# Performance work log

Hardware: AMD Instinct MI355X
Metric: run time of the kernel (lower is better)

The kernel has to match this reference:

```python
import jax, jax.numpy as jnp
from jax import lax
import numpy as np

B, H, W = 2, 48, 48
C_IN, C_OUT = 96, 192
D_INNER, N_STATE, DT_RANK, K = 192, 16, 6, 4  # VMamba: expand=2, d_state=16, dt_rank=ceil(C/16)
EPS = 1e-5


def setup_inputs() -> dict:
    ks = jax.random.split(jax.random.key(0), 16)
    s = 0.02
    r = lambda k, sh, sc=s: jax.random.normal(k, sh, jnp.float32) * sc
    d, N, R = D_INNER, N_STATE, DT_RANK
    return {
        "x": jax.random.normal(ks[0], (B, C_IN, H, W), jnp.float32),
        "ln_g": jnp.ones((C_IN,), jnp.float32),
        "ln_b": jnp.zeros((C_IN,), jnp.float32),
        "in_proj_w": r(ks[1], (2 * d, C_IN)),
        "dwconv_w": r(ks[2], (d, 1, 3, 3)),
        "dwconv_b": jnp.zeros((d,), jnp.float32),
        "x_proj_w": r(ks[3], (K, R + 2 * N, d)),
        "dt_w": r(ks[4], (K, d, R)),
        "dt_b": r(ks[5], (K, d), 0.1),
        "A_logs": jnp.tile(jnp.log(jnp.arange(1, N + 1, dtype=jnp.float32)), (K, d, 1)),
        "Ds": jnp.ones((K, d), jnp.float32),
        "out_norm_g": jnp.ones((d,), jnp.float32),
        "out_norm_b": jnp.zeros((d,), jnp.float32),
        "out_proj_w": r(ks[6], (C_IN, d)),
        "w1": r(ks[7], (C_OUT, C_IN, 1, 1)),
        "b1": jnp.zeros((C_OUT,), jnp.float32),
        "w31": r(ks[8], (C_OUT, C_IN, 3, 3)),
        "b31": jnp.zeros((C_OUT,), jnp.float32),
        "w32": r(ks[9], (C_OUT, C_IN, 3, 3)),
        "b32": jnp.zeros((C_OUT,), jnp.float32),
        "w33": r(ks[10], (C_OUT, C_OUT, 3, 3)),
        "b33": jnp.zeros((C_OUT,), jnp.float32),
        "bn_g": jnp.ones((3 * C_OUT,), jnp.float32),
        "bn_b": jnp.zeros((3 * C_OUT,), jnp.float32),
        "bn_m": r(ks[11], (3 * C_OUT,), 0.1),
        "bn_v": jax.random.uniform(ks[12], (3 * C_OUT,), jnp.float32) + 0.5,
        "prelu_a": jnp.float32(0.25),
    }


def _layernorm(x, g, b):
    m = jnp.mean(x, -1, keepdims=True)
    v = jnp.var(x, -1, keepdims=True)
    return (x - m) * lax.rsqrt(v + EPS) * g + b


def _conv(x, w, b, stride, pad, groups=1):
    y = lax.conv_general_dilated(x, w, (stride, stride), [(pad, pad), (pad, pad)],
                                 dimension_numbers=("NCHW", "OIHW", "NCHW"),
                                 feature_group_count=groups)
    return y + b[None, :, None, None]


def _ss2d(x, in_proj_w, dwconv_w, dwconv_b, x_proj_w, dt_w, dt_b, A_logs, Ds,
          out_norm_g, out_norm_b, out_proj_w):
    # x: (B, H, W, C)
    Bb, Hh, Ww, C = x.shape
    d, N, R = D_INNER, N_STATE, DT_RANK
    L = Hh * Ww
    xz = jnp.einsum("bhwc,ec->bhwe", x, in_proj_w)  # (B,H,W,2d)
    xin, z = jnp.split(xz, 2, axis=-1)
    xc = jnp.transpose(xin, (0, 3, 1, 2))           # (B,d,H,W)
    xc = jax.nn.silu(_conv(xc, dwconv_w, dwconv_b, 1, 1, groups=d))
    # 4 scan directions: row-major, col-major, and their reverses
    x_flat = xc.reshape(Bb, d, L)
    x_t = jnp.transpose(xc, (0, 1, 3, 2)).reshape(Bb, d, L)
    xs = jnp.stack([x_flat, x_t, x_flat[:, :, ::-1], x_t[:, :, ::-1]], axis=1)  # (B,K,d,L)
    x_dbl = jnp.einsum("bkdl,kcd->bkcl", xs, x_proj_w)
    dts, Bs, Cs = x_dbl[:, :, :R], x_dbl[:, :, R:R + N], x_dbl[:, :, R + N:]
    delta = jax.nn.softplus(jnp.einsum("bkrl,kdr->bkdl", dts, dt_w) + dt_b[None, :, :, None])
    A = -jnp.exp(A_logs)                                   # (K,d,N)
    dA = jnp.exp(jnp.einsum("bkdl,kdn->lbkdn", delta, A))  # (L,B,K,d,N)
    dBu = jnp.einsum("bkdl,bknl,bkdl->lbkdn", delta, Bs, xs)
    Cseq = jnp.transpose(Cs, (3, 0, 1, 2))                 # (L,B,K,N)

    def step(h, inp):
        dA_t, dBu_t, c_t = inp
        h = dA_t * h + dBu_t
        return h, jnp.einsum("bkdn,bkn->bkd", h, c_t)

    h0 = jnp.zeros((Bb, K, d, N), x.dtype)
    _, ys = lax.scan(step, h0, (dA, dBu, Cseq))            # ys: (L,B,K,d)
    ys = jnp.transpose(ys, (1, 2, 3, 0)) + xs * Ds[None, :, :, None]  # (B,K,d,L)

    def t_back(a):  # undo the HW transpose of col-major scans
        return jnp.transpose(a.reshape(Bb, d, Ww, Hh), (0, 1, 3, 2)).reshape(Bb, d, L)

    y = ys[:, 0] + ys[:, 2, :, ::-1] + t_back(ys[:, 1]) + t_back(ys[:, 3, :, ::-1])
    y = _layernorm(jnp.transpose(y, (0, 2, 1)), out_norm_g, out_norm_b).reshape(Bb, Hh, Ww, d)
    y = y * jax.nn.silu(z)
    return jnp.einsum("bhwd,cd->bhwc", y, out_proj_w)


def reference(x, ln_g, ln_b, in_proj_w, dwconv_w, dwconv_b, x_proj_w, dt_w, dt_b,
              A_logs, Ds, out_norm_g, out_norm_b, out_proj_w,
              w1, b1, w31, b31, w32, b32, w33, b33,
              bn_g, bn_b, bn_m, bn_v, prelu_a):
    # VSSBlock: residual + SS2D on LayerNorm'd NHWC features
    x_nhwc = jnp.transpose(x, (0, 2, 3, 1))
    x_nhwc = x_nhwc + _ss2d(_layernorm(x_nhwc, ln_g, ln_b), in_proj_w, dwconv_w,
                            dwconv_b, x_proj_w, dt_w, dt_b, A_logs, Ds,
                            out_norm_g, out_norm_b, out_proj_w)
    xm = jnp.transpose(x_nhwc, (0, 3, 1, 2))  # (B,C,H,W)
    # multi-branch stride-2 downsample
    x1 = _conv(xm, w1, b1, 2, 0)
    x2 = _conv(xm, w31, b31, 2, 1)
    x3 = _conv(_conv(xm, w32, b32, 2, 1), w33, b33, 1, 1)
    out = jnp.concatenate([x1, x2, x3], axis=1)  # (B, 3*C_OUT, H/2, W/2)
    # BatchNorm2d (inference, running stats) + PReLU(single param)
    out = (out - bn_m[None, :, None, None]) * lax.rsqrt(bn_v + EPS)[None, :, None, None] \
          * bn_g[None, :, None, None] + bn_b[None, :, None, None]
    return jnp.where(out > 0, out, prelu_a * out)
```

## Files before the change

### kernel.cpp

```cpp
#include <hip/hip_runtime.h>
#include <math.h>

#define BB_ 2
#define HH 48
#define WW 48
#define LL 2304
#define CIN 96
#define DD 192
#define KK 4
#define NN 16
#define RR 6
#define NCH 96
#define LC 24
#define COUT 192
#define OH 24
#define OW 24
#define OHW 576
#define NPX 1152
#define NTOT 4608
#define EPSF 1e-5f

typedef __attribute__((ext_vector_type(8))) short bf16x8;
typedef __attribute__((ext_vector_type(4))) float f32x4;

__device__ __forceinline__ short f2bf(float f) {
  unsigned u = __float_as_uint(f);
  unsigned r = (u + 0x7fffu + ((u >> 16) & 1u)) >> 16;
  return (short)r;
}

__global__ __launch_bounds__(256) void k_prep(const float* __restrict__ x,
                                              const float* __restrict__ g,
                                              const float* __restrict__ b,
                                              const float* __restrict__ inw,
                                              const float* __restrict__ xpw,
                                              const float* __restrict__ w31,
                                              const float* __restrict__ w32,
                                              const float* __restrict__ w33,
                                              const float* __restrict__ w1,
                                              const float* __restrict__ wout,
                                              float* __restrict__ stats,
                                              float* __restrict__ WgT,
                                              float* __restrict__ sWg,
                                              float* __restrict__ sWb,
                                              short* __restrict__ At3p,
                                              short* __restrict__ At1b,
                                              short* __restrict__ At2b,
                                              short* __restrict__ woutb) {
  int bx = blockIdx.x;
  int tid = threadIdx.x;
  if (bx < 72) {
    int bb = bx / 36; int l0 = (bx % 36) * 64;
    int p = tid >> 2, q = tid & 3;
    int l = l0 + p;
    const float* xp = x + bb * CIN * LL + l;
    float s = 0.f, ss = 0.f;
    for (int c = q; c < CIN; c += 4) { float v = xp[c * LL]; s += v; ss += v * v; }
    s += __shfl_xor(s, 1, 64); s += __shfl_xor(s, 2, 64);
    ss += __shfl_xor(ss, 1, 64); ss += __shfl_xor(ss, 2, 64);
    if (q == 0) {
      float m = s / CIN; float var = ss / CIN - m * m;
      stats[(bb * LL + l) * 2 + 0] = m;
      stats[(bb * LL + l) * 2 + 1] = rsqrtf(var + EPSF);
    }
  } else if (bx == 72) {
    for (int e = tid; e < 2 * DD; e += 256) {
      float swg = 0.f, swb = 0.f;
      for (int c = 0; c < CIN; c++) {
        float w = inw[e * CIN + c];
        float wg = w * g[c];
        WgT[c * 384 + e] = wg;
        swg += wg; swb += w * b[c];
      }
      sWg[e] = swg; sWb[e] = swb;
    }
  } else if (bx < 217) {
    int idx = (bx - 73) * 256 + tid;
    if (idx < 4 * 48 * 192) {
      int m = idx / 192, d = idx - m * 192;
      int kd = m / 48, r = m - kd * 48;
      At3p[idx] = (r < 38) ? f2bf(xpw[(kd * 38 + r) * 192 + d]) : (short)0;
    }
  } else if (bx < 2161) {
    int i = (bx - 217) * 256 + tid;
    if (i < 497664) {
      float v;
      if (i < 165888) v = w31[i];
      else if (i < 331776) v = w32[i - 165888];
      else {
        int k = i % 864; int m = i / 864 - 384;
        v = (k % 9 == 4) ? w1[m * 96 + k / 9] : 0.f;
      }
      At1b[i] = f2bf(v);
    }
  } else if (bx < 3457) {
    int i = (bx - 2161) * 256 + tid;
    if (i < 331776) At2b[i] = f2bf(w33[i]);
  } else {
    int i = (bx - 3457) * 256 + tid;
    if (i < 18432) woutb[i] = f2bf(wout[i]);
  }
}

__global__ __launch_bounds__(256) void k_dwconv(const float* __restrict__ xin,
                                                const float* __restrict__ wdw,
                                                const float* __restrict__ bdw,
                                                float* __restrict__ xs,
                                                short* __restrict__ xsb) {
  __shared__ float vt[32 * 50];
  int bid = blockIdx.x;
  int bb = bid / 288; int r = bid % 288; int dg = r / 72; int tile = r % 72;
  int l0 = tile * 32;
  int d0 = dg * 48;
  for (int i = threadIdx.x; i < 32 * 48; i += 256) {
    int lj = i & 31, dl = i >> 5;
    int d = d0 + dl;
    int l = l0 + lj;
    int h = l / WW, w = l % WW;
    const float* xp = xin + (bb * DD + d) * LL;
    const float* wq = wdw + d * 9;
    float acc = bdw[d];
#pragma unroll
    for (int kh = 0; kh < 3; kh++) {
      int ih = h + kh - 1; if (ih < 0 || ih >= HH) continue;
#pragma unroll
      for (int kw = 0; kw < 3; kw++) {
        int iw = w + kw - 1; if (iw < 0 || iw >= WW) continue;
        acc += xp[ih * WW + iw] * wq[kh * 3 + kw];
      }
    }
    float v = acc / (1.f + __expf(-acc));
    vt[lj * 50 + dl] = v;
  }
  __syncthreads();
  for (int j = threadIdx.x; j < 32 * 48; j += 256) {
    int lj = j / 48, dl = j - lj * 48;
    int d = d0 + dl;
    int l = l0 + lj;
    int h = l / WW, w = l % WW;
    int lt = w * HH + h;
    float v = vt[lj * 50 + dl];
    xs[((size_t)(bb * 2 + 0) * LL + l) * DD + d] = v;
    xs[((size_t)(bb * 2 + 1) * LL + lt) * DD + d] = v;
    xsb[((size_t)bb * LL + l) * DD + d] = f2bf(v);
  }
}

__global__ __launch_bounds__(256) void k_xprojF(const short* __restrict__ At3p,
                                                const short* __restrict__ xsb,
                                                const float* __restrict__ dtw,
                                                const float* __restrict__ dtb,
                                                float* __restrict__ Bsb,
                                                float* __restrict__ Csb,
                                                float* __restrict__ delta) {
  __shared__ short As[48][40];
  __shared__ short Bs[64][40];
  __shared__ float ct[38][65];
  int bid = blockIdx.x;
  int kd = bid / 72; int tile = bid % 72;
  int pg0 = tile * 64;
  int bb = pg0 / LL;
  int lbase = pg0 - bb * LL;
  int tid = threadIdx.x;
  int lane = tid & 63;
  int wvn = tid >> 6;
  int row16 = lane & 15;
  int kg = lane >> 4;
  f32x4 acc[3];
#pragma unroll
  for (int j = 0; j < 3; j++) acc[j] = (f32x4){0.f, 0.f, 0.f, 0.f};
  int sm = tid >> 2, sk8 = (tid & 3) * 8;
  for (int ks = 0; ks < 192; ks += 32) {
    if (tid < 192)
      *(bf16x8*)&As[sm][sk8] =
          *(const bf16x8*)&At3p[(size_t)(kd * 48 + sm) * 192 + ks + sk8];
    *(bf16x8*)&Bs[sm][sk8] =
        *(const bf16x8*)&xsb[(size_t)(pg0 + sm) * 192 + ks + sk8];
    __syncthreads();
    bf16x8 b = *(const bf16x8*)&Bs[wvn * 16 + row16][kg * 8];
#pragma unroll
    for (int j = 0; j < 3; j++) {
      bf16x8 a = *(const bf16x8*)&As[j * 16 + row16][kg * 8];
      acc[j] = __builtin_amdgcn_mfma_f32_16x16x32_bf16(a, b, acc[j], 0, 0, 0);
    }
    __syncthreads();
  }
#pragma unroll
  for (int j = 0; j < 3; j++) {
    int rowb = j * 16 + kg * 4;
    int col = wvn * 16 + row16;
#pragma unroll
    for (int i = 0; i < 4; i++)
      if (rowb + i < 38) ct[rowb + i][col] = acc[j][i];
  }
  __syncthreads();
  for (int i = tid; i < 64 * 16; i += 256) {
    int lj = i >> 4, n = i & 15;
    int l = lbase + lj; int h = l / WW, w = l - h * WW; int lt = w * HH + h;
    int pos = (kd == 0) ? l : (kd == 1) ? lt : (kd == 2) ? (LL - 1 - l) : (LL - 1 - lt);
    size_t base = ((size_t)(bb * 4 + kd) * LL + pos) * NN + n;
    Bsb[base] = ct[6 + n][lj];
    Csb[base] = ct[22 + n][lj];
  }
  for (int i = tid; i < 64 * 192; i += 256) {
    int lj = i / 192, d = i - lj * 192;
    int l = lbase + lj; int h = l / WW, w = l - h * WW; int lt = w * HH + h;
    int pos = (kd == 0) ? l : (kd == 1) ? lt : (kd == 2) ? (LL - 1 - l) : (LL - 1 - lt);
    const float* wd = dtw + (kd * DD + d) * RR;
    float a2 = dtb[kd * DD + d];
#pragma unroll
    for (int r = 0; r < RR; r++) a2 += wd[r] * ct[r][lj];
    float sp = a2 > 20.f ? a2 : log1pf(__expf(a2));
    delta[((size_t)(bb * 4 + kd) * LL + pos) * DD + d] = sp;
  }
}

__global__ __launch_bounds__(192) void k_scan1(const float* __restrict__ delta,
                                               const float* __restrict__ xs,
                                               const float* __restrict__ Bsb,
                                               const float* __restrict__ A_logs,
                                               float* __restrict__ Pbuf,
                                               float* __restrict__ Sbuf) {
  __shared__ float Bls[LC * NN];
  int bid = blockIdx.x;
  int c = bid % NCH; int bk = bid / NCH; int k = bk & 3; int bb = bk >> 2;
  int t0 = c * LC;
  int d = threadIdx.x;
  const float* bp = Bsb + ((size_t)bk * LL + t0) * NN;
  for (int i = d; i < LC * NN; i += 192) Bls[i] = bp[i];
  float A[NN];
  {
    const float4* ap = (const float4*)(A_logs + (k * DD + d) * NN);
#pragma unroll
    for (int j = 0; j < 4; j++) {
      float4 a4 = ap[j];
      A[4 * j + 0] = -__expf(a4.x); A[4 * j + 1] = -__expf(a4.y);
      A[4 * j + 2] = -__expf(a4.z); A[4 * j + 3] = -__expf(a4.w);
    }
  }
  bool seq = true;
#pragma unroll
  for (int n = 0; n < NN; n++) seq = seq && (fabsf(A[n] + (float)(n + 1)) < 1e-3f);
  float h[NN];
#pragma unroll
  for (int n = 0; n < NN; n++) h[n] = 0.f;
  float sd = 0.f;
  __syncthreads();
  const float* dp = delta + ((size_t)bk * LL + t0) * DD + d;
  const float* xpb = xs + ((size_t)(bb * 2 + (k & 1)) * LL) * DD + d;
  const float* xp; int xstep;
  if (k < 2) { xp = xpb + (size_t)t0 * DD; xstep = DD; }
  else       { xp = xpb + (size_t)(LL - 1 - t0) * DD; xstep = -DD; }
#pragma unroll 2
  for (int t = 0; t < LC; ++t) {
    float dt = dp[t * DD];
    float xv = xp[t * xstep];
    float u = dt * xv;
    sd += dt;
    float dA[NN];
    if (seq) {
      float q = __expf(-dt);
      float q2 = q * q, q4 = q2 * q2, q8 = q4 * q4;
      dA[0] = q; dA[1] = q2; dA[2] = q2 * q; dA[3] = q4;
      dA[4] = q4 * q; dA[5] = q4 * q2; dA[6] = q4 * dA[2]; dA[7] = q8;
      dA[8] = q8 * q; dA[9] = q8 * q2; dA[10] = q8 * dA[2]; dA[11] = q8 * q4;
      dA[12] = q8 * dA[4]; dA[13] = q8 * dA[5]; dA[14] = q8 * dA[6]; dA[15] = q8 * q8;
    } else {
#pragma unroll
      for (int n = 0; n < NN; n++) dA[n] = __expf(dt * A[n]);
    }
    const float4* b4 = (const float4*)&Bls[t * NN];
#pragma unroll
    for (int j = 0; j < 4; j++) {
      float4 bv = b4[j];
      h[4 * j + 0] = dA[4 * j + 0] * h[4 * j + 0] + u * bv.x;
      h[4 * j + 1] = dA[4 * j + 1] * h[4 * j + 1] + u * bv.y;
      h[4 * j + 2] = dA[4 * j + 2] * h[4 * j + 2] + u * bv.z;
      h[4 * j + 3] = dA[4 * j + 3] * h[4 * j + 3] + u * bv.w;
    }
  }
  int chn = (bk * DD + d) * NN;
  float* pp = Pbuf + (size_t)c * 24576 + chn;
  float* sp = Sbuf + (size_t)c * 24576 + chn;
#pragma unroll
  for (int n = 0; n < NN; n++) { pp[n] = __expf(A[n] * sd); sp[n] = h[n]; }
}

__global__ __launch_bounds__(256) void k_scan2(const float* __restrict__ Pbuf,
                                               const float* __restrict__ Sbuf,
                                               float* __restrict__ Hinit) {
  int idx = blockIdx.x * 256 + threadIdx.x;
  float h = 0.f;
  for (int c = 0; c < NCH; c++) {
    Hinit[(size_t)c * 24576 + idx] = h;
    h = Pbuf[(size_t)c * 24576 + idx] * h + Sbuf[(size_t)c * 24576 + idx];
  }
}

__global__ __launch_bounds__(192) void k_scan3(const float* __restrict__ delta,
                                               const float* __restrict__ xs,
                                               const float* __restrict__ Bsb,
                                               const float* __restrict__ Csb,
                                               const float* __restrict__ A_logs,
                                               const float* __restrict__ Ds,
                                               const float* __restrict__ Hinit,
                                               float* __restrict__ ys) {
  __shared__ float Bls[LC * NN];
  __shared__ float Cls[LC * NN];
  int bid = blockIdx.x;
  int c = bid % NCH; int bk = bid / NCH; int k = bk & 3; int bb = bk >> 2;
  int t0 = c * LC;
  int d = threadIdx.x;
  const float* bp = Bsb + ((size_t)bk * LL + t0) * NN;
  const float* cp = Csb + ((size_t)bk * LL + t0) * NN;
  for (int i = d; i < LC * NN; i += 192) { Bls[i] = bp[i]; Cls[i] = cp[i]; }
  float A[NN];
  {
    const float4* ap = (const float4*)(A_logs + (k * DD + d) * NN);
#pragma unroll
    for (int j = 0; j < 4; j++) {
      float4 a4 = ap[j];
      A[4 * j + 0] = -__expf(a4.x); A[4 * j + 1] = -__expf(a4.y);
      A[4 * j + 2] = -__expf(a4.z); A[4 * j + 3] = -__expf(a4.w);
    }
  }
  bool seq = true;
#pragma unroll
  for (int n = 0; n < NN; n++) seq = seq && (fabsf(A[n] + (float)(n + 1)) < 1e-3f);
  float Dv = Ds[k * DD + d];
  float h[NN];
  {
    const float4* hp = (const float4*)(Hinit + (size_t)c * 24576 + (bk * DD + d) * NN);
#pragma unroll
    for (int j = 0; j < 4; j++) {
      float4 h4 = hp[j];
      h[4 * j + 0] = h4.x; h[4 * j + 1] = h4.y;
      h[4 * j + 2] = h4.z; h[4 * j + 3] = h4.w;
    }
  }
  __syncthreads();
  const float* dp = delta + ((size_t)bk * LL + t0) * DD + d;
  const float* xpb = xs + ((size_t)(bb * 2 + (k & 1)) * LL) * DD + d;
  const float* xp; int xstep;
  if (k < 2) { xp = xpb + (size_t)t0 * DD; xstep = DD; }
  else       { xp = xpb + (size_t)(LL - 1 - t0) * DD; xstep = -DD; }
  float* yp = ys + ((size_t)bk * LL + t0) * DD + d;
#pragma unroll 2
  for (int t = 0; t < LC; ++t) {
    float dt = dp[t * DD];
    float xv = xp[t * xstep];
    float u = dt * xv;
    float y = 0.f;
    float dA[NN];
    if (seq) {
      float q = __expf(-dt);
      float q2 = q * q, q4 = q2 * q2, q8 = q4 * q4;
      dA[0] = q; dA[1] = q2; dA[2] = q2 * q; dA[3] = q4;
      dA[4] = q4 * q; dA[5] = q4 * q2; dA[6] = q4 * dA[2]; dA[7] = q8;
      dA[8] = q8 * q; dA[9] = q8 * q2; dA[10] = q8 * dA[2]; dA[11] = q8 * q4;
      dA[12] = q8 * dA[4]; dA[13] = q8 * dA[5]; dA[14] = q8 * dA[6]; dA[15] = q8 * q8;
    } else {
#pragma unroll
      for (int n = 0; n < NN; n++) dA[n] = __expf(dt * A[n]);
    }
    const float4* b4 = (const float4*)&Bls[t * NN];
    const float4* c4 = (const float4*)&Cls[t * NN];
#pragma unroll
    for (int j = 0; j < 4; j++) {
      float4 bv = b4[j];
      float4 cc = c4[j];
      h[4 * j + 0] = dA[4 * j + 0] * h[4 * j + 0] + u * bv.x;
      h[4 * j + 1] = dA[4 * j + 1] * h[4 * j + 1] + u * bv.y;
      h[4 * j + 2] = dA[4 * j + 2] * h[4 * j + 2] + u * bv.z;
      h[4 * j + 3] = dA[4 * j + 3] * h[4 * j + 3] + u * bv.w;
      y += h[4 * j + 0] * cc.x + h[4 * j + 1] * cc.y
         + h[4 * j + 2] * cc.z + h[4 * j + 3] * cc.w;
    }
    yp[t * DD] = y + Dv * xv;
  }
}

__global__ __launch_bounds__(256) void k_combineF(const float* __restrict__ ys,
                                                  const float* __restrict__ z,
                                                  const float* __restrict__ ong,
                                                  const float* __restrict__ onb,
                                                  const short* __restrict__ Wbf,
                                                  const float* __restrict__ x,
                                                  float* __restrict__ xm) {
  __shared__ float yt[32 * 194];
  __shared__ unsigned Wlu[96 * 98];
  int bx = blockIdx.x; int bb = bx / 72; int l0 = (bx % 72) * 32;
  int tid = threadIdx.x;
  const unsigned* Wu = (const unsigned*)Wbf;
  for (int i = tid; i < 96 * 96; i += 256) {
    int e = i / 96, d2 = i - e * 96;
    Wlu[e * 98 + d2] = Wu[i];
  }
  for (int i = tid; i < 32 * DD; i += 256) {
    int p = i / DD, d = i - p * DD;
    int l = l0 + p; int h = l / WW, w = l - h * WW;
    int t1 = w * HH + h;
    float v = ys[(((size_t)bb * KK + 0) * LL + l) * DD + d]
            + ys[(((size_t)bb * KK + 1) * LL + t1) * DD + d]
            + ys[(((size_t)bb * KK + 2) * LL + (LL - 1 - l)) * DD + d]
            + ys[(((size_t)bb * KK + 3) * LL + (LL - 1 - t1)) * DD + d];
    yt[p * 194 + d] = v;
  }
  __syncthreads();
  int p = tid >> 3, q = tid & 7;
  int l = l0 + p;
  float s = 0.f, ss = 0.f;
  for (int d = q * 24; d < q * 24 + 24; d++) { float v = yt[p * 194 + d]; s += v; ss += v * v; }
  s += __shfl_xor(s, 1, 64); s += __shfl_xor(s, 2, 64); s += __shfl_xor(s, 4, 64);
  ss += __shfl_xor(ss, 1, 64); ss += __shfl_xor(ss, 2, 64); ss += __shfl_xor(ss, 4, 64);
  float m = s / DD, var = ss / DD - m * m;
  float rr = rsqrtf(var + EPSF);
  const float* zp = z + (bb * LL + l) * DD;
  for (int d = q * 24; d < q * 24 + 24; d++) {
    float v = (yt[p * 194 + d] - m) * rr * ong[d] + onb[d];
    float zv = zp[d];
    yt[p * 194 + d] = v * zv / (1.f + __expf(-zv));
  }
  __syncthreads();
  float acc[12];
#pragma unroll
  for (int j = 0; j < 12; j++) acc[j] = 0.f;
  for (int d2 = 0; d2 < 96; d2++) {
    float2 y2 = *(float2*)&yt[p * 194 + 2 * d2];
#pragma unroll
    for (int j = 0; j < 12; j++) {
      unsigned wv = Wlu[(q * 12 + j) * 98 + d2];
      float wlo = __uint_as_float(wv << 16);
      float whi = __uint_as_float(wv & 0xffff0000u);
      acc[j] += y2.x * wlo + y2.y * whi;
    }
  }
#pragma unroll
  for (int j = 0; j < 12; j++) {
    int e = q * 12 + j;
    size_t off = ((size_t)bb * CIN + e) * LL + l;
    xm[off] = x[off] + acc[j];
  }
}

template<int MT, int KTOT, int KCHUNK, int CI, int IH, int STRIDE>
__global__ __launch_bounds__(256) void k_cgemm_mfma(const short* __restrict__ Abf,
                                                    const float* __restrict__ SRC,
                                                    float* __restrict__ Cout) {
  __shared__ short As[64][40];
  __shared__ short Bs[64][40];
  int n0 = blockIdx.x * 64;
  int m0 = blockIdx.y * 64;
  int kz = blockIdx.z;
  int k0 = kz * KCHUNK;
  int tid = threadIdx.x;
  int lane = tid & 63;
  int wv = tid >> 6;
  int row16 = lane & 15;
  int kg = lane >> 4;
  int sm = tid >> 2;
  int sk8 = (tid & 3) * 8;
  int n = n0 + sm;
  int bb = n / OHW; int rem = n - bb * OHW;
  int oh = rem / OW, ow = rem - oh * OW;
  f32x4 acc[4];
#pragma unroll
  for (int i = 0; i < 4; i++) acc[i] = (f32x4){0.f, 0.f, 0.f, 0.f};
  for (int ks = 0; ks < KCHUNK; ks += 32) {
    *(bf16x8*)&As[sm][sk8] =
        *(const bf16x8*)&Abf[(size_t)(m0 + sm) * KTOT + k0 + ks + sk8];
    bf16x8 bvv;
#pragma unroll
    for (int j = 0; j < 8; j++) {
      int k = k0 + ks + sk8 + j;
      int ci = k / 9; int r9 = k - ci * 9;
      int kh = r9 / 3, kw = r9 - kh * 3;
      int ih = STRIDE * oh + kh - 1;
      int iw = STRIDE * ow + kw - 1;
      float v = (ih >= 0 && ih < IH && iw >= 0 && iw < IH)
              ? SRC[((size_t)(bb * CI + ci) * IH + ih) * IH + iw] : 0.f;
      bvv[j] = f2bf(v);
    }
    *(bf16x8*)&Bs[sm][sk8] = bvv;
    __syncthreads();
    bf16x8 a = *(const bf16x8*)&As[wv * 16 + row16][kg * 8];
#pragma unroll
    for (int tn = 0; tn < 4; tn++) {
      bf16x8 b = *(const bf16x8*)&Bs[tn * 16 + row16][kg * 8];
      acc[tn] = __builtin_amdgcn_mfma_f32_16x16x32_bf16(a, b, acc[tn], 0, 0, 0);
    }
    __syncthreads();
  }
#pragma unroll
  for (int tn = 0; tn < 4; tn++) {
    int col = n0 + tn * 16 + row16;
    int rowb = m0 + wv * 16 + kg * 4;
#pragma unroll
    for (int i = 0; i < 4; i++)
      Cout[((size_t)kz * MT + rowb + i) * NPX + col] = acc[tn][i];
  }
}

template<int MT, int KD>
__global__ __launch_bounds__(256) void k_gemmF(const float* __restrict__ At,
                                               const float* __restrict__ Bm,
                                               int ldb, int boffB,
                                               float* __restrict__ C0,
                                               int ldc, int boffC,
                                               const float* __restrict__ a0,
                                               const float* __restrict__ a1,
                                               const float* __restrict__ a2,
                                               float* __restrict__ a3) {
  __shared__ float As[16][64];
  __shared__ float Bs[16][64];
  int n0 = blockIdx.x * 64;
  int m0 = blockIdx.y * 64;
  int bb = blockIdx.z;
  const float* B = Bm + (size_t)bb * boffB;
  int tid = threadIdx.x;
  int lr = tid >> 4;
  int lc = (tid & 15) * 4;
  int tm = tid >> 4;
  int tn = tid & 15;
  float acc[4][4] = {};
  for (int ks = 0; ks < KD; ks += 16) {
    *(float4*)&As[lr][lc] = *(const float4*)&At[(ks + lr) * MT + m0 + lc];
    *(float4*)&Bs[lr][lc] = *(const float4*)&B[(size_t)(ks + lr) * ldb + n0 + lc];
    __syncthreads();
#pragma unroll
    for (int kk = 0; kk < 16; kk++) {
      float4 a = *(float4*)&As[kk][tm * 4];
      float4 b = *(float4*)&Bs[kk][tn * 4];
      acc[0][0] += a.x * b.x; acc[0][1] += a.x * b.y; acc[0][2] += a.x * b.z; acc[0][3] += a.x * b.w;
      acc[1][0] += a.y * b.x; acc[1][1] += a.y * b.y; acc[1][2] += a.y * b.z; acc[1][3] += a.y * b.w;
      acc[2][0] += a.z * b.x; acc[2][1] += a.z * b.y; acc[2][2] += a.z * b.z; acc[2][3] += a.z * b.w;
      acc[3][0] += a.w * b.x; acc[3][1] += a.w * b.y; acc[3][2] += a.w * b.z; acc[3][3] += a.w * b.w;
    }
    __syncthreads();
  }
  int n = n0 + tn * 4;
  float m_[4], r_[4];
#pragma unroll
  for (int j = 0; j < 4; j++) {
    m_[j] = a0[((size_t)bb * LL + n + j) * 2];
    r_[j] = a0[((size_t)bb * LL + n + j) * 2 + 1];
  }
#pragma unroll
  for (int i = 0; i < 4; i++) {
    int e = m0 + tm * 4 + i;
    float swg = a1[e], swb = a2[e];
    float v0 = r_[0] * (acc[i][0] - m_[0] * swg) + swb;
    float v1 = r_[1] * (acc[i][1] - m_[1] * swg) + swb;
    float v2 = r_[2] * (acc[i][2] - m_[2] * swg) + swb;
    float v3 = r_[3] * (acc[i][3] - m_[3] * swg) + swb;
    if (e < DD) {
      float4 v = {v0, v1, v2, v3};
      *(float4*)&C0[(size_t)bb * boffC + (size_t)e * ldc + n] = v;
    } else {
      a3[((size_t)bb * LL + n + 0) * DD + (e - DD)] = v0;
      a3[((size_t)bb * LL + n + 1) * DD + (e - DD)] = v1;
      a3[((size_t)bb * LL + n + 2) * DD + (e - DD)] = v2;
      a3[((size_t)bb * LL + n + 3) * DD + (e - DD)] = v3;
    }
  }
}

__global__ __launch_bounds__(256) void k_reduce1(const float* __restrict__ Cp1,
                                                 const float* __restrict__ b1,
                                                 const float* __restrict__ b31,
                                                 const float* __restrict__ b32,
                                                 const float* __restrict__ bn_g,
                                                 const float* __restrict__ bn_b,
                                                 const float* __restrict__ bn_m,
                                                 const float* __restrict__ bn_v,
                                                 const float* __restrict__ prelu_a,
                                                 float* __restrict__ out,
                                                 float* __restrict__ t3) {
  int idx = blockIdx.x * 256 + threadIdx.x;
  if (idx >= 576 * NPX) return;
  int m = idx / NPX, n = idx % NPX;
  float s = 0.f;
#pragma unroll
  for (int c = 0; c < 3; c++) s += Cp1[(size_t)c * 576 * NPX + idx];
  int bb = n / OHW, o = n % OHW;
  if (m < 192) {
    s += b31[m];
    int cc = 192 + m;
    float scale = rsqrtf(bn_v[cc] + EPSF) * bn_g[cc];
    float v = s * scale + (bn_b[cc] - bn_m[cc] * scale);
    float a = prelu_a[0];
    out[((size_t)bb * 576 + cc) * OHW + o] = v > 0.f ? v : a * v;
  } else if (m < 384) {
    s += b32[m - 192];
    t3[((size_t)bb * COUT + (m - 192)) * OHW + o] = s;
  } else {
    s += b1[m - 384];
    int cc = m - 384;
    float scale = rsqrtf(bn_v[cc] + EPSF) * bn_g[cc];
    float v = s * scale + (bn_b[cc] - bn_m[cc] * scale);
    float a = prelu_a[0];
    out[((size_t)bb * 576 + cc) * OHW + o] = v > 0.f ? v : a * v;
  }
}

__global__ __launch_bounds__(256) void k_reduce2(const float* __restrict__ Cp2,
                                                 const float* __restrict__ b33,
                                                 const float* __restrict__ bn_g,
                                                 const float* __restrict__ bn_b,
                                                 const float* __restrict__ bn_m,
                                                 const float* __restrict__ bn_v,
                                                 const float* __restrict__ prelu_a,
                                                 float* __restrict__ out) {
  int idx = blockIdx.x * 256 + threadIdx.x;
  if (idx >= 192 * NPX) return;
  int m = idx / NPX, n = idx % NPX;
  float s = b33[m];
#pragma unroll
  for (int c = 0; c < 6; c++) s += Cp2[(size_t)c * 192 * NPX + idx];
  int bb = n / OHW, o = n % OHW;
  int cc = 384 + m;
  float scale = rsqrtf(bn_v[cc] + EPSF) * bn_g[cc];
  float v = s * scale + (bn_b[cc] - bn_m[cc] * scale);
  float a = prelu_a[0];
  out[((size_t)bb * 576 + cc) * OHW + o] = v > 0.f ? v : a * v;
}

extern "C" void kernel_launch(void* const* d_in, const int* in_sizes, int n_in,
                              void* d_out, int out_size, void* d_ws, size_t ws_size,
                              hipStream_t stream) {
  const float* x        = (const float*)d_in[0];
  const float* ln_g     = (const float*)d_in[1];
  const float* ln_b     = (const float*)d_in[2];
  const float* in_proj_w= (const float*)d_in[3];
  const float* dwconv_w = (const float*)d_in[4];
  const float* dwconv_b = (const float*)d_in[5];
  const float* x_proj_w = (const float*)d_in[6];
  const float* dt_w     = (const float*)d_in[7];
  const float* dt_b     = (const float*)d_in[8];
  const float* A_logs   = (const float*)d_in[9];
  const float* Ds       = (const float*)d_in[10];
  const float* out_norm_g = (const float*)d_in[11];
  const float* out_norm_b = (const float*)d_in[12];
  const float* out_proj_w = (const float*)d_in[13];
  const float* w1  = (const float*)d_in[14];
  const float* b1  = (const float*)d_in[15];
  const float* w31 = (const float*)d_in[16];
  const float* b31 = (const float*)d_in[17];
  const float* w32 = (const float*)d_in[18];
  const float* b32 = (const float*)d_in[19];
  const float* w33 = (const float*)d_in[20];
  const float* b33 = (const float*)d_in[21];
  const float* bn_g = (const float*)d_in[22];
  const float* bn_b = (const float*)d_in[23];
  const float* bn_m = (const float*)d_in[24];
  const float* bn_v = (const float*)d_in[25];
  const float* prelu_a = (const float*)d_in[26];

  float* ws = (float*)d_ws;
  float* stats = ws + 0;
  float* WgT   = ws + 16384;
  float* sWg   = ws + 65536;
  float* sWb   = ws + 66048;
  short* At3p  = (short*)(ws + 98304);
  short* At1b  = (short*)(ws + 147456);
  short* At2b  = (short*)(ws + 397312);
  short* woutb = (short*)(ws + 565248);
  float* xin   = ws + 2097152;
  float* z     = ws + 3145728;
  float* xs    = ws + 4194304;
  short* xsb   = (short*)(ws + 6291456);
  float* delta = ws + 10485760;
  float* Bsb   = ws + 14155776;
  float* Csb   = ws + 14680064;
  float* Pbuf  = ws + 15728640;
  float* Sbuf  = ws + 18874368;
  float* Hinit = ws + 22020096;
  float* ys    = ws + 25165824;
  float* xm    = ws + 29360128;
  float* t3    = ws + 30408704;
  float* Cp1   = ws + 31457280;
  float* Cp2   = ws + 33554432;
  float* out = (float*)d_out;

  k_prep<<<3529, 256, 0, stream>>>(x, ln_g, ln_b, in_proj_w, x_proj_w,
                                   w31, w32, w33, w1, out_proj_w,
                                   stats, WgT, sWg, sWb, At3p, At1b, At2b, woutb);
  k_gemmF<384, 96><<<dim3(36, 6, 2), 256, 0, stream>>>(
      WgT, x, LL, CIN * LL, xin, LL, DD * LL, stats, sWg, sWb, z);
  k_dwconv<<<576, 256, 0, stream>>>(xin, dwconv_w, dwconv_b, xs, xsb);
  k_xprojF<<<288, 256, 0, stream>>>(At3p, xsb, dt_w, dt_b, Bsb, Csb, delta);
  k_scan1<<<768, 192, 0, stream>>>(delta, xs, Bsb, A_logs, Pbuf, Sbuf);
  k_scan2<<<96, 256, 0, stream>>>(Pbuf, Sbuf, Hinit);
  k_scan3<<<768, 192, 0, stream>>>(delta, xs, Bsb, Csb, A_logs, Ds, Hinit, ys);
  k_combineF<<<144, 256, 0, stream>>>(ys, z, out_norm_g, out_norm_b, woutb, x, xm);
  k_cgemm_mfma<576, 864, 288, CIN, HH, 2><<<dim3(18, 9, 3), 256, 0, stream>>>(
      At1b, xm, Cp1);
  k_reduce1<<<2592, 256, 0, stream>>>(Cp1, b1, b31, b32, bn_g, bn_b, bn_m, bn_v,
                                      prelu_a, out, t3);
  k_cgemm_mfma<192, 1728, 288, COUT, OH, 1><<<dim3(18, 3, 6), 256, 0, stream>>>(
      At2b, t3, Cp2);
  k_reduce2<<<864, 256, 0, stream>>>(Cp2, b33, bn_g, bn_b, bn_m, bn_v, prelu_a, out);
}
```

Before: 190.7 us.

## Move in_proj to bf16 MFMA, halve combine tile, unroll chunk scan

Replaces the fp32 SIMT in_proj GEMM with a bf16 MFMA kernel. The weights are stored as bf16 and the prep kernel gains extra blocks that transpose x to pixel-major bf16. The combine kernel now uses 16-pixel tiles, doubling its grid to 288 blocks for better occupancy. The inter-chunk scan loop is unrolled by 4. Rounding in_proj inputs to bf16 lowers precision, and the extra transpose pass costs memory traffic.

Measured after the change: 190.7 us. Within noise of the previous version (-0.0%).

```diff
diff --git a/kernel.cpp b/kernel.cpp
--- a/kernel.cpp
+++ b/kernel.cpp
@@ -40,13 +40,15 @@
                                               const float* __restrict__ w1,
                                               const float* __restrict__ wout,
                                               float* __restrict__ stats,
-                                              float* __restrict__ WgT,
+                                              short* __restrict__ WgTb,
                                               float* __restrict__ sWg,
                                               float* __restrict__ sWb,
                                               short* __restrict__ At3p,
                                               short* __restrict__ At1b,
                                               short* __restrict__ At2b,
-                                              short* __restrict__ woutb) {
+                                              short* __restrict__ woutb,
+                                              short* __restrict__ xb) {
+  __shared__ float tile[32][33];
   int bx = blockIdx.x;
   int tid = threadIdx.x;
   if (bx < 72) {
@@ -69,7 +71,7 @@
       for (int c = 0; c < CIN; c++) {
         float w = inw[e * CIN + c];
         float wg = w * g[c];
-        WgT[c * 384 + e] = wg;
+        WgTb[e * CIN + c] = f2bf(wg);
         swg += wg; swb += w * b[c];
       }
       sWg[e] = swg; sWb[e] = swb;
@@ -96,9 +98,70 @@
   } else if (bx < 3457) {
     int i = (bx - 2161) * 256 + tid;
     if (i < 331776) At2b[i] = f2bf(w33[i]);
-  } else {
+  } else if (bx < 3529) {
     int i = (bx - 3457) * 256 + tid;
     if (i < 18432) woutb[i] = f2bf(wout[i]);
+  } else {
+    int tt = bx - 3529;
+    int bb = tt / 216; int r2 = tt % 216;
+    int ct = r2 / 72, lt = r2 % 72;
+    int c0 = ct * 32, l0 = lt * 32;
+    int r = tid >> 5, cc = tid & 31;
+    for (int rr = r; rr < 32; rr += 8)
+      tile[rr][cc] = x[(size_t)bb * CIN * LL + (c0 + rr) * LL + l0 + cc];
+    __syncthreads();
+    for (int rr = r; rr < 32; rr += 8)
+      xb[((size_t)bb * LL + l0 + rr) * CIN + c0 + cc] = f2bf(tile[cc][rr]);
+  }
+}
+
+__global__ __launch_bounds__(256) void k_inprojM(const short* __restrict__ WgTb,
+                                                 const short* __restrict__ xb,
+                                                 const float* __restrict__ stats,
+                                                 const float* __restrict__ sWg,
+                                                 const float* __restrict__ sWb,
+                                                 float* __restrict__ xin,
+                                                 float* __restrict__ z) {
+  __shared__ short As[64][40];
+  __shared__ short Bs[64][40];
+  int n0 = blockIdx.x * 64;
+  int m0 = blockIdx.y * 64;
+  int tid = threadIdx.x;
+  int lane = tid & 63;
+  int wv = tid >> 6;
+  int row16 = lane & 15;
+  int kg = lane >> 4;
+  int sm = tid >> 2;
+  int sk8 = (tid & 3) * 8;
+  f32x4 acc[4];
+#pragma unroll
+  for (int i = 0; i < 4; i++) acc[i] = (f32x4){0.f, 0.f, 0.f, 0.f};
+#pragma unroll
+  for (int ks = 0; ks < 96; ks += 32) {
+    *(bf16x8*)&As[sm][sk8] = *(const bf16x8*)&WgTb[(size_t)(m0 + sm) * CIN + ks + sk8];
+    *(bf16x8*)&Bs[sm][sk8] = *(const bf16x8*)&xb[(size_t)(n0 + sm) * CIN + ks + sk8];
+    __syncthreads();
+    bf16x8 a = *(const bf16x8*)&As[wv * 16 + row16][kg * 8];
+#pragma unroll
+    for (int tn = 0; tn < 4; tn++) {
+      bf16x8 b = *(const bf16x8*)&Bs[tn * 16 + row16][kg * 8];
+      acc[tn] = __builtin_amdgcn_mfma_f32_16x16x32_bf16(a, b, acc[tn], 0, 0, 0);
+    }
+    __syncthreads();
+  }
+#pragma unroll
+  for (int tn = 0; tn < 4; tn++) {
+    int px = n0 + tn * 16 + row16;
+    int bb = px / LL, l = px - bb * LL;
+    float mm = stats[px * 2], rr = stats[px * 2 + 1];
+    int rowb = m0 + wv * 16 + kg * 4;
+#pragma unroll
+    for (int i = 0; i < 4; i++) {
+      int e = rowb + i;
+      float v = rr * (acc[tn][i] - mm * sWg[e]) + sWb[e];
+      if (e < DD) xin[((size_t)bb * DD + e) * LL + l] = v;
+      else z[(size_t)px * DD + (e - DD)] = v;
+    }
   }
 }
 
@@ -291,6 +354,7 @@
                                                float* __restrict__ Hinit) {
   int idx = blockIdx.x * 256 + threadIdx.x;
   float h = 0.f;
+#pragma unroll 4
   for (int c = 0; c < NCH; c++) {
     Hinit[(size_t)c * 24576 + idx] = h;
     h = Pbuf[(size_t)c * 24576 + idx] * h + Sbuf[(size_t)c * 24576 + idx];
@@ -387,16 +451,16 @@
                                                   const short* __restrict__ Wbf,
                                                   const float* __restrict__ x,
                                                   float* __restrict__ xm) {
-  __shared__ float yt[32 * 194];
+  __shared__ float yt[16 * 194];
   __shared__ unsigned Wlu[96 * 98];
-  int bx = blockIdx.x; int bb = bx / 72; int l0 = (bx % 72) * 32;
+  int bx = blockIdx.x; int bb = bx / 144; int l0 = (bx % 144) * 16;
   int tid = threadIdx.x;
   const unsigned* Wu = (const unsigned*)Wbf;
   for (int i = tid; i < 96 * 96; i += 256) {
     int e = i / 96, d2 = i - e * 96;
     Wlu[e * 98 + d2] = Wu[i];
   }
-  for (int i = tid; i < 32 * DD; i += 256) {
+  for (int i = tid; i < 16 * DD; i += 256) {
     int p = i / DD, d = i - p * DD;
     int l = l0 + p; int h = l / WW, w = l - h * WW;
     int t1 = w * HH + h;
@@ -407,37 +471,39 @@
     yt[p * 194 + d] = v;
   }
   __syncthreads();
-  int p = tid >> 3, q = tid & 7;
+  int p = tid >> 4, q = tid & 15;
   int l = l0 + p;
   float s = 0.f, ss = 0.f;
-  for (int d = q * 24; d < q * 24 + 24; d++) { float v = yt[p * 194 + d]; s += v; ss += v * v; }
-  s += __shfl_xor(s, 1, 64); s += __shfl_xor(s, 2, 64); s += __shfl_xor(s, 4, 64);
-  ss += __shfl_xor(ss, 1, 64); ss += __shfl_xor(ss, 2, 64); ss += __shfl_xor(ss, 4, 64);
+  for (int d = q * 12; d < q * 12 + 12; d++) { float v = yt[p * 194 + d]; s += v; ss += v * v; }
+  s += __shfl_xor(s, 1, 64); s += __shfl_xor(s, 2, 64);
+  s += __shfl_xor(s, 4, 64); s += __shfl_xor(s, 8, 64);
+  ss += __shfl_xor(ss, 1, 64); ss += __shfl_xor(ss, 2, 64);
+  ss += __shfl_xor(ss, 4, 64); ss += __shfl_xor(ss, 8, 64);
   float m = s / DD, var = ss / DD - m * m;
   float rr = rsqrtf(var + EPSF);
-  const float* zp = z + (bb * LL + l) * DD;
-  for (int d = q * 24; d < q * 24 + 24; d++) {
+  const float* zp = z + (size_t)(bb * LL + l) * DD;
+  for (int d = q * 12; d < q * 12 + 12; d++) {
     float v = (yt[p * 194 + d] - m) * rr * ong[d] + onb[d];
     float zv = zp[d];
     yt[p * 194 + d] = v * zv / (1.f + __expf(-zv));
   }
   __syncthreads();
-  float acc[12];
-#pragma unroll
-  for (int j = 0; j < 12; j++) acc[j] = 0.f;
+  float acc[6];
+#pragma unroll
+  for (int j = 0; j < 6; j++) acc[j] = 0.f;
   for (int d2 = 0; d2 < 96; d2++) {
     float2 y2 = *(float2*)&yt[p * 194 + 2 * d2];
 #pragma unroll
-    for (int j = 0; j < 12; j++) {
-      unsigned wv = Wlu[(q * 12 + j) * 98 + d2];
+    for (int j = 0; j < 6; j++) {
+      unsigned wv = Wlu[(q * 6 + j) * 98 + d2];
       float wlo = __uint_as_float(wv << 16);
       float whi = __uint_as_float(wv & 0xffff0000u);
       acc[j] += y2.x * wlo + y2.y * whi;
     }
   }
 #pragma unroll
-  for (int j = 0; j < 12; j++) {
-    int e = q * 12 + j;
+  for (int j = 0; j < 6; j++) {
+    int e = q * 6 + j;
     size_t off = ((size_t)bb * CIN + e) * LL + l;
     xm[off] = x[off] + acc[j];
   }
@@ -498,70 +564,6 @@
 #pragma unroll
     for (int i = 0; i < 4; i++)
       Cout[((size_t)kz * MT + rowb + i) * NPX + col] = acc[tn][i];
-  }
-}
-
-template<int MT, int KD>
-__global__ __launch_bounds__(256) void k_gemmF(const float* __restrict__ At,
-                                               const float* __restrict__ Bm,
-                                               int ldb, int boffB,
-                                               float* __restrict__ C0,
-                                               int ldc, int boffC,
-                                               const float* __restrict__ a0,
-                                               const float* __restrict__ a1,
-                                               const float* __restrict__ a2,
-                                               float* __restrict__ a3) {
-  __shared__ float As[16][64];
-  __shared__ float Bs[16][64];
-  int n0 = blockIdx.x * 64;
-  int m0 = blockIdx.y * 64;
-  int bb = blockIdx.z;
-  const float* B = Bm + (size_t)bb * boffB;
-  int tid = threadIdx.x;
-  int lr = tid >> 4;
-  int lc = (tid & 15) * 4;
-  int tm = tid >> 4;
-  int tn = tid & 15;
-  float acc[4][4] = {};
-  for (int ks = 0; ks < KD; ks += 16) {
-    *(float4*)&As[lr][lc] = *(const float4*)&At[(ks + lr) * MT + m0 + lc];
-    *(float4*)&Bs[lr][lc] = *(const float4*)&B[(size_t)(ks + lr) * ldb + n0 + lc];
-    __syncthreads();
-#pragma unroll
-    for (int kk = 0; kk < 16; kk++) {
-      float4 a = *(float4*)&As[kk][tm * 4];
-      float4 b = *(float4*)&Bs[kk][tn * 4];
-      acc[0][0] += a.x * b.x; acc[0][1] += a.x * b.y; acc[0][2] += a.x * b.z; acc[0][3] += a.x * b.w;
-      acc[1][0] += a.y * b.x; acc[1][1] += a.y * b.y; acc[1][2] += a.y * b.z; acc[1][3] += a.y * b.w;
-      acc[2][0] += a.z * b.x; acc[2][1] += a.z * b.y; acc[2][2] += a.z * b.z; acc[2][3] += a.z * b.w;
-      acc[3][0] += a.w * b.x; acc[3][1] += a.w * b.y; acc[3][2] += a.w * b.z; acc[3][3] += a.w * b.w;
-    }
-    __syncthreads();
-  }
-  int n = n0 + tn * 4;
-  float m_[4], r_[4];
-#pragma unroll
-  for (int j = 0; j < 4; j++) {
-    m_[j] = a0[((size_t)bb * LL + n + j) * 2];
-    r_[j] = a0[((size_t)bb * LL + n + j) * 2 + 1];
-  }
-#pragma unroll
-  for (int i = 0; i < 4; i++) {
-    int e = m0 + tm * 4 + i;
-    float swg = a1[e], swb = a2[e];
-    float v0 = r_[0] * (acc[i][0] - m_[0] * swg) + swb;
-    float v1 = r_[1] * (acc[i][1] - m_[1] * swg) + swb;
-    float v2 = r_[2] * (acc[i][2] - m_[2] * swg) + swb;
-    float v3 = r_[3] * (acc[i][3] - m_[3] * swg) + swb;
-    if (e < DD) {
-      float4 v = {v0, v1, v2, v3};
-      *(float4*)&C0[(size_t)bb * boffC + (size_t)e * ldc + n] = v;
-    } else {
-      a3[((size_t)bb * LL + n + 0) * DD + (e - DD)] = v0;
-      a3[((size_t)bb * LL + n + 1) * DD + (e - DD)] = v1;
-      a3[((size_t)bb * LL + n + 2) * DD + (e - DD)] = v2;
-      a3[((size_t)bb * LL + n + 3) * DD + (e - DD)] = v3;
-    }
   }
 }
 
@@ -658,7 +660,7 @@
 
   float* ws = (float*)d_ws;
   float* stats = ws + 0;
-  float* WgT   = ws + 16384;
+  short* WgTb  = (short*)(ws + 16384);
   float* sWg   = ws + 65536;
   float* sWb   = ws + 66048;
   short* At3p  = (short*)(ws + 98304);
@@ -680,19 +682,20 @@
   float* t3    = ws + 30408704;
   float* Cp1   = ws + 31457280;
   float* Cp2   = ws + 33554432;
+  short* xb    = (short*)(ws + 35651584);
   float* out = (float*)d_out;
 
-  k_prep<<<3529, 256, 0, stream>>>(x, ln_g, ln_b, in_proj_w, x_proj_w,
+  k_prep<<<3961, 256, 0, stream>>>(x, ln_g, ln_b, in_proj_w, x_proj_w,
                                    w31, w32, w33, w1, out_proj_w,
-                                   stats, WgT, sWg, sWb, At3p, At1b, At2b, woutb);
-  k_gemmF<384, 96><<<dim3(36, 6, 2), 256, 0, stream>>>(
-      WgT, x, LL, CIN * LL, xin, LL, DD * LL, stats, sWg, sWb, z);
+                                   stats, WgTb, sWg, sWb, At3p, At1b, At2b,
+                                   woutb, xb);
+  k_inprojM<<<dim3(72, 6), 256, 0, stream>>>(WgTb, xb, stats, sWg, sWb, xin, z);
   k_dwconv<<<576, 256, 0, stream>>>(xin, dwconv_w, dwconv_b, xs, xsb);
   k_xprojF<<<288, 256, 0, stream>>>(At3p, xsb, dt_w, dt_b, Bsb, Csb, delta);
   k_scan1<<<768, 192, 0, stream>>>(delta, xs, Bsb, A_logs, Pbuf, Sbuf);
   k_scan2<<<96, 256, 0, stream>>>(Pbuf, Sbuf, Hinit);
   k_scan3<<<768, 192, 0, stream>>>(delta, xs, Bsb, Csb, A_logs, Ds, Hinit, ys);
-  k_combineF<<<144, 256, 0, stream>>>(ys, z, out_norm_g, out_norm_b, woutb, x, xm);
+  k_combineF<<<288, 256, 0, stream>>>(ys, z, out_norm_g, out_norm_b, woutb, x, xm);
   k_cgemm_mfma<576, 864, 288, CIN, HH, 2><<<dim3(18, 9, 3), 256, 0, stream>>>(
       At1b, xm, Cp1);
   k_reduce1<<<2592, 256, 0, stream>>>(Cp1, b1, b31, b32, bn_g, bn_b, bn_m, bn_v,
```
